# Kernel tuning notes

Hardware: AMD Instinct MI355X
Metric: run time of the kernel (lower is better)

The kernel has to match this reference:

```python
import jax, jax.numpy as jnp
import numpy as np

N_MAPS = 6          # n: maps per class (5 kernels + 1 text)
N_CLASSES = 2       # len(text_classify)
RATIO = 3
LAMBDA = 0.7
EPS = 1e-4
NEG_INF = -1e30


def setup_inputs() -> dict:
    key = jax.random.key(0)
    k1, k2, k3 = jax.random.split(key, 3)
    B, C, H, W = 8, N_CLASSES * N_MAPS, 640, 640
    outputs = jax.random.normal(k1, (B, C, H, W), dtype=jnp.float32)
    labels = jax.random.uniform(k2, (B, C, H, W), dtype=jnp.float32)
    training_mask = jax.random.uniform(k3, (B, 1, H, W), dtype=jnp.float32)
    return {"outputs": outputs, "labels": labels, "training_mask": training_mask}


def _dice_loss(pred, target, mask):
    # pred/target: (B, HW) or (B, K, HW); mask broadcastable. sums over last axis.
    p = jax.nn.sigmoid(pred) * mask
    t = target * mask
    a = jnp.sum(p * t, axis=-1)
    b = jnp.sum(p * p, axis=-1) + EPS
    c = jnp.sum(t * t, axis=-1) + EPS
    return 1.0 - 2.0 * a / (b + c)


def _ohem_single(score, gt, tm):
    # score/gt/tm: (H, W). Returns float32 (H, W) selection mask.
    pos_num = jnp.sum((gt > 0.5) & (tm > 0.5))
    neg = gt <= 0.5
    neg_total = jnp.sum(neg)
    neg_num = jnp.minimum(pos_num * RATIO, neg_total)
    # descending sort of negative-position scores
    neg_sorted = -jnp.sort(-jnp.where(neg, score, NEG_INF).ravel())
    thr = neg_sorted[jnp.clip(neg_num - 1, 0, score.size - 1)]
    sel = ((score >= thr) | (gt > 0.5)) & (tm > 0.5)
    fallback = (pos_num == 0) | (neg_num == 0)
    return jnp.where(fallback, tm, sel.astype(jnp.float32))


def reference(outputs, labels, training_mask):
    B, C, H, W = outputs.shape
    tm = training_mask[:, 0]  # (B, H, W)
    text_losses, kernel_losses, class_losses = [], [], []
    for i in range(N_CLASSES):
        texts = outputs[:, (i + 1) * N_MAPS - 1]                 # (B, H, W)
        kernels = outputs[:, i * N_MAPS:(i + 1) * N_MAPS - 1]    # (B, K, H, W)
        gt_texts = labels[:, (i + 1) * N_MAPS - 1]
        gt_kernels = labels[:, i * N_MAPS:(i + 1) * N_MAPS - 1]
        # OHEM mask (detached in original via numpy round-trip)
        sel_text = jax.lax.stop_gradient(jax.vmap(_ohem_single)(texts, gt_texts, tm))
        loss_text = _dice_loss(texts.reshape(B, -1), gt_texts.reshape(B, -1),
                               sel_text.reshape(B, -1))  # (B,)
        # kernel mask: (sigmoid(texts) > 0.5) & (tm > 0.5), detached
        sel_k = jax.lax.stop_gradient(
            ((jax.nn.sigmoid(texts) > 0.5) & (tm > 0.5)).astype(jnp.float32))
        K = gt_kernels.shape[1]
        loss_kernels = _dice_loss(kernels.reshape(B, K, -1),
                                  gt_kernels.reshape(B, K, -1),
                                  sel_k.reshape(B, 1, -1))  # (B, K) per-kernel losses
        loss_kernels = jnp.mean(loss_kernels, axis=1)  # mean over kernels -> (B,)
        lt = jnp.mean(loss_text)      # reduction='mean'
        lk = jnp.mean(loss_kernels)
        loss = LAMBDA * lt + (1.0 - LAMBDA) * lk
        text_losses.append(lt)
        kernel_losses.append(lk)
        class_losses.append(loss)
    muti_class_loss_avg = jnp.mean(jnp.stack(class_losses))
    text_loss_avg = jnp.mean(jnp.stack(text_losses))
    kernel_loss_avg = jnp.mean(jnp.stack(kernel_losses))
    # stacked as (3,): [muti_class_loss_avg, text_loss_avg, kernel_loss_avg]
    return jnp.stack([muti_class_loss_avg, text_loss_avg, kernel_loss_avg])
```

## Files before the change

kernel.cpp:

```cpp
#include <hip/hip_runtime.h>

#define HW 409600
#define NCH 12

#define OFF_TACC   0
#define OFF_KACC   256
#define OFF_TFAST  1280
#define OFF_TFB    1536
#define OFF_POSF   1792
#define OFF_NEGF   1856
#define OFF_DONE   1920
#define OFF_NEGNUM 1984
#define OFF_SEL1   2048
#define OFF_KREM1  2112
#define OFF_SEL2   2176
#define OFF_KREM2  2240
#define OFF_THR    2304
#define OFF_HA     4096
#define OFF_HB     (OFF_HA + 16*2048*4)
#define OFF_HC     (OFF_HB + 16*2048*4)
#define OFF_META_END (OFF_HC + 16*1024*4)
#define OFF_MASK   ((OFF_META_END + 255) & ~255)

__device__ __forceinline__ unsigned flipkey(float x){
  unsigned b = __float_as_uint(x);
  return (b & 0x80000000u) ? ~b : (b | 0x80000000u);
}
__device__ __forceinline__ float unflip(unsigned u){
  unsigned b = (u & 0x80000000u) ? (u ^ 0x80000000u) : ~u;
  return __uint_as_float(b);
}

__device__ __forceinline__ float sigm(float x){
  return __fdividef(1.0f, 1.0f + __expf(-x));
}

__global__ __launch_bounds__(256) void k_main(
    const float* __restrict__ outputs, const float* __restrict__ labels,
    const float* __restrict__ tmask, unsigned char* __restrict__ maskb,
    float* __restrict__ posF, float* __restrict__ negF,
    float* __restrict__ tfastA, float* __restrict__ tfbA,
    float* __restrict__ kaccA)
{
  int img = blockIdx.x / 200;
  int blk = blockIdx.x % 200;
  int ci = img >> 3, bi = img & 7;
  const float* ob = outputs + (size_t)(bi*NCH + ci*6)*HW;
  const float* lb = labels  + (size_t)(bi*NCH + ci*6)*HW;
  const float* mp = tmask   + (size_t)bi*HW;
  unsigned char* mw = maskb + (size_t)img*HW;

  float ka0=0,ka1=0,ka2=0,ka3=0,ka4=0;
  float kb0=0,kb1=0,kb2=0,kb3=0,kb4=0;
  float kc0=0,kc1=0,kc2=0,kc3=0,kc4=0;
  float af=0,bf=0,cf=0;
  float ab_=0,bb_=0,cb_=0;
  unsigned pos=0, neg=0;

  #pragma unroll
  for (int it=0; it<2; it++){
    int px = blk*2048 + it*1024 + (int)threadIdx.x*4;
    float4 ov0 = *(const float4*)(ob + 0*HW + px);
    float4 ov1 = *(const float4*)(ob + 1*HW + px);
    float4 ov2 = *(const float4*)(ob + 2*HW + px);
    float4 ov3 = *(const float4*)(ob + 3*HW + px);
    float4 ov4 = *(const float4*)(ob + 4*HW + px);
    float4 ov5 = *(const float4*)(ob + 5*HW + px);
    float4 lv0 = *(const float4*)(lb + 0*HW + px);
    float4 lv1 = *(const float4*)(lb + 1*HW + px);
    float4 lv2 = *(const float4*)(lb + 2*HW + px);
    float4 lv3 = *(const float4*)(lb + 3*HW + px);
    float4 lv4 = *(const float4*)(lb + 4*HW + px);
    float4 lv5 = *(const float4*)(lb + 5*HW + px);
    float4 mv  = *(const float4*)(mp + px);

    float oo[6][4] = {{ov0.x,ov0.y,ov0.z,ov0.w},{ov1.x,ov1.y,ov1.z,ov1.w},
                      {ov2.x,ov2.y,ov2.z,ov2.w},{ov3.x,ov3.y,ov3.z,ov3.w},
                      {ov4.x,ov4.y,ov4.z,ov4.w},{ov5.x,ov5.y,ov5.z,ov5.w}};
    float ll[6][4] = {{lv0.x,lv0.y,lv0.z,lv0.w},{lv1.x,lv1.y,lv1.z,lv1.w},
                      {lv2.x,lv2.y,lv2.z,lv2.w},{lv3.x,lv3.y,lv3.z,lv3.w},
                      {lv4.x,lv4.y,lv4.z,lv4.w},{lv5.x,lv5.y,lv5.z,lv5.w}};
    float tmv[4] = {mv.x,mv.y,mv.z,mv.w};
    unsigned char mby[4];

    #pragma unroll
    for (int c=0;c<4;c++){
      float t  = oo[5][c];
      float g  = ll[5][c];
      float tm = tmv[c];
      bool tpos  = (tm > 0.5f);
      bool isneg = (g <= 0.5f);
      bool selk  = (t > 0.0f) && tpos;
      pos += (unsigned)((!isneg) && tpos);
      neg += (unsigned)isneg;
      mby[c] = (unsigned char)((selk?1u:0u)|(tpos?2u:0u)|(isneg?4u:0u));

      float s5 = sigm(t);
      float mf = tpos ? 1.0f : 0.0f;
      af += mf * (s5*g);
      bf += mf * (s5*s5);
      cf += mf * (g*g);
      float pfb = s5*tm, tfb = g*tm;
      ab_ += pfb*tfb; bb_ += pfb*pfb; cb_ += tfb*tfb;
      float mk = selk ? 1.0f : 0.0f;
      {
        float s, l;
        s = sigm(oo[0][c]); l = ll[0][c];
        ka0 += mk*(s*l); kb0 += mk*(s*s); kc0 += mk*(l*l);
        s = sigm(oo[1][c]); l = ll[1][c];
        ka1 += mk*(s*l); kb1 += mk*(s*s); kc1 += mk*(l*l);
        s = sigm(oo[2][c]); l = ll[2][c];
        ka2 += mk*(s*l); kb2 += mk*(s*s); kc2 += mk*(l*l);
        s = sigm(oo[3][c]); l = ll[3][c];
        ka3 += mk*(s*l); kb3 += mk*(s*s); kc3 += mk*(l*l);
        s = sigm(oo[4][c]); l = ll[4][c];
        ka4 += mk*(s*l); kb4 += mk*(s*s); kc4 += mk*(l*l);
      }
    }
    *(uchar4*)(mw + px) = make_uchar4(mby[0],mby[1],mby[2],mby[3]);
  }

  float red[23] = {af,bf,cf, ab_,bb_,cb_,
                   ka0,kb0,kc0, ka1,kb1,kc1, ka2,kb2,kc2,
                   ka3,kb3,kc3, ka4,kb4,kc4,
                   (float)pos, (float)neg};
  #pragma unroll
  for (int k=0;k<23;k++){
    #pragma unroll
    for (int o=32;o;o>>=1) red[k] += __shfl_down(red[k],o,64);
  }
  __shared__ float sred[4][23];
  int wv = threadIdx.x >> 6, ln = threadIdx.x & 63;
  if (ln==0){
    #pragma unroll
    for (int k=0;k<23;k++) sred[wv][k] = red[k];
  }
  __syncthreads();
  int t = threadIdx.x;
  if (t < 23){
    float v = sred[0][t]+sred[1][t]+sred[2][t]+sred[3][t];
    float* dst;
    if      (t < 3)  dst = tfastA + img*3 + t;
    else if (t < 6)  dst = tfbA   + img*3 + (t-3);
    else if (t < 21) dst = kaccA  + img*15 + (t-6);
    else if (t ==21) dst = posF + img;
    else             dst = negF + img;
    atomicAdd(dst, v);
  }
}

__global__ void k_decide(
    const float* __restrict__ posF, const float* __restrict__ negF,
    const float* __restrict__ tfastA, const float* __restrict__ tfbA,
    float* __restrict__ tacc, unsigned* __restrict__ doneA,
    unsigned* __restrict__ negnumA, float* __restrict__ thrA)
{
  int img = threadIdx.x;
  if (img >= 16) return;
  float pos = posF[img], negt = negF[img];
  float nn = fminf(pos*3.0f, negt);
  bool fb   = (pos == 0.0f) || (nn == 0.0f);
  bool fast = (!fb) && (nn == negt);
  thrA[img] = 0.0f;
  if (fb || fast){
    doneA[img] = 1u; negnumA[img] = 1u;
    const float* src = fb ? (tfbA + img*3) : (tfastA + img*3);
    tacc[img*3+0] = src[0];
    tacc[img*3+1] = src[1];
    tacc[img*3+2] = src[2];
  } else {
    doneA[img] = 0u;
    negnumA[img] = (unsigned)(nn + 0.5f);
  }
}


__global__ __launch_bounds__(256) void k_hista(
    const float* __restrict__ outputs, const unsigned char* __restrict__ maskb,
    const unsigned* __restrict__ doneA, unsigned* __restrict__ histA)
{
  int img = blockIdx.x / 50;
  if (doneA[img]) return;
  int blk = blockIdx.x % 50;
  int ci = img>>3, bi = img&7;
  const float* tp = outputs + (size_t)(bi*NCH + ci*6 + 5)*HW;
  const unsigned char* mk = maskb + (size_t)img*HW;
  __shared__ unsigned lh[2048];
  for (int j=threadIdx.x; j<2048; j+=256) lh[j]=0u;
  __syncthreads();
  #pragma unroll
  for (int it=0; it<8; it++){
    int px = blk*8192 + it*1024 + (int)threadIdx.x*4;
    float4 tv = *(const float4*)(tp+px);
    uchar4 mq = *(const uchar4*)(mk+px);
    float tt[4]={tv.x,tv.y,tv.z,tv.w};
    unsigned char ma[4]={mq.x,mq.y,mq.z,mq.w};
    #pragma unroll
    for (int c=0;c<4;c++)
      if (ma[c] & 4) atomicAdd(&lh[flipkey(tt[c]) >> 21], 1u);
  }
  __syncthreads();
  unsigned* gh = histA + (size_t)img*2048u;
  for (int j=threadIdx.x; j<2048; j+=256){
    unsigned v = lh[j];
    if (v) atomicAdd(&gh[j], v);
  }
}

template<int NB>
__device__ void scan_desc(const unsigned* h, unsigned k, unsigned* selOut, unsigned* kremOut)
{
  const int PER = NB/256;
  int t = threadIdx.x;
  unsigned s=0;
  #pragma unroll
  for (int j=0;j<PER;j++) s += h[t*PER+j];
  __shared__ unsigned cs[256];
  cs[t]=s; __syncthreads();
  if (t==0){
    unsigned cum=0, ch=0, kin=k;
    for (int c=255;c>=0;c--){
      if (cum + cs[c] >= k){ ch=(unsigned)c; kin=k-cum; break; }
      cum += cs[c];
    }
    unsigned cum2=0, sel=ch*PER, kr=1;
    for (int x=PER-1;x>=0;x--){
      unsigned v = h[ch*PER+x];
      cum2 += v;
      if (cum2 >= kin){ sel=ch*PER+(unsigned)x; kr = kin - (cum2 - v); break; }
    }
    *selOut = sel; *kremOut = kr;
  }
}

__global__ __launch_bounds__(256) void k_scan_a(
    const unsigned* __restrict__ histA, const unsigned* __restrict__ doneA,
    const unsigned* __restrict__ negnumA, unsigned* __restrict__ sel1A,
    unsigned* __restrict__ krem1A)
{
  int img = blockIdx.x;
  if (doneA[img]) return;
  scan_desc<2048>(histA + (size_t)img*2048u, negnumA[img], &sel1A[img], &krem1A[img]);
}

__global__ __launch_bounds__(256) void k_histb(
    const float* __restrict__ outputs, const unsigned char* __restrict__ maskb,
    const unsigned* __restrict__ sel1A, const unsigned* __restrict__ doneA,
    unsigned* __restrict__ histB)
{
  int img = blockIdx.x / 50;
  if (doneA[img]) return;
  int blk = blockIdx.x % 50;
  int ci = img>>3, bi = img&7;
  unsigned sel1 = sel1A[img];
  const float* tp = outputs + (size_t)(bi*NCH + ci*6 + 5)*HW;
  const unsigned char* mk = maskb + (size_t)img*HW;
  __shared__ unsigned lh[2048];
  for (int j=threadIdx.x; j<2048; j+=256) lh[j]=0u;
  __syncthreads();
  #pragma unroll
  for (int it=0; it<8; it++){
    int px = blk*8192 + it*1024 + (int)threadIdx.x*4;
    float4 tv = *(const float4*)(tp+px);
    uchar4 mq = *(const uchar4*)(mk+px);
    float tt[4]={tv.x,tv.y,tv.z,tv.w};
    unsigned char ma[4]={mq.x,mq.y,mq.z,mq.w};
    #pragma unroll
    for (int c=0;c<4;c++){
      if (ma[c] & 4){
        unsigned key = flipkey(tt[c]);
        if ((key>>21) == sel1) atomicAdd(&lh[(key>>10) & 0x7FFu], 1u);
      }
    }
  }
  __syncthreads();
  unsigned* gh = histB + (size_t)img*2048u;
  for (int j=threadIdx.x; j<2048; j+=256){
    unsigned v = lh[j];
    if (v) atomicAdd(&gh[j], v);
  }
}

__global__ __launch_bounds__(256) void k_scan_b(
    const unsigned* __restrict__ histB, const unsigned* __restrict__ krem1A,
    const unsigned* __restrict__ doneA, unsigned* __restrict__ sel2A,
    unsigned* __restrict__ krem2A)
{
  int img = blockIdx.x;
  if (doneA[img]) return;
  scan_desc<2048>(histB + (size_t)img*2048u, krem1A[img], &sel2A[img], &krem2A[img]);
}

__global__ __launch_bounds__(256) void k_histc(
    const float* __restrict__ outputs, const unsigned char* __restrict__ maskb,
    const unsigned* __restrict__ sel1A, const unsigned* __restrict__ sel2A,
    const unsigned* __restrict__ doneA, unsigned* __restrict__ histC)
{
  int img = blockIdx.x / 50;
  if (doneA[img]) return;
  int blk = blockIdx.x % 50;
  int ci = img>>3, bi = img&7;
  unsigned p22 = (sel1A[img]<<11) | sel2A[img];
  const float* tp = outputs + (size_t)(bi*NCH + ci*6 + 5)*HW;
  const unsigned char* mk = maskb + (size_t)img*HW;
  __shared__ unsigned lh[1024];
  for (int j=threadIdx.x; j<1024; j+=256) lh[j]=0u;
  __syncthreads();
  #pragma unroll
  for (int it=0; it<8; it++){
    int px = blk*8192 + it*1024 + (int)threadIdx.x*4;
    float4 tv = *(const float4*)(tp+px);
    uchar4 mq = *(const uchar4*)(mk+px);
    float tt[4]={tv.x,tv.y,tv.z,tv.w};
    unsigned char ma[4]={mq.x,mq.y,mq.z,mq.w};
    #pragma unroll
    for (int c=0;c<4;c++){
      if (ma[c] & 4){
        unsigned key = flipkey(tt[c]);
        if ((key>>10) == p22) atomicAdd(&lh[key & 0x3FFu], 1u);
      }
    }
  }
  __syncthreads();
  unsigned* gh = histC + (size_t)img*1024u;
  for (int j=threadIdx.x; j<1024; j+=256){
    unsigned v = lh[j];
    if (v) atomicAdd(&gh[j], v);
  }
}

__global__ __launch_bounds__(256) void k_scan_c(
    const unsigned* __restrict__ histC, const unsigned* __restrict__ sel1A,
    const unsigned* __restrict__ sel2A, const unsigned* __restrict__ krem2A,
    const unsigned* __restrict__ doneA, float* __restrict__ thrA)
{
  int img = blockIdx.x;
  if (doneA[img]) return;
  __shared__ unsigned sel3, kr;
  scan_desc<1024>(histC + (size_t)img*1024u, krem2A[img], &sel3, &kr);
  __syncthreads();
  if (threadIdx.x==0){
    unsigned key = (sel1A[img]<<21) | (sel2A[img]<<10) | sel3;
    thrA[img] = unflip(key);
  }
}

__global__ __launch_bounds__(256) void k_dtext(
    const float* __restrict__ outputs, const float* __restrict__ labels,
    const unsigned char* __restrict__ maskb, const unsigned* __restrict__ doneA,
    const float* __restrict__ thrA, float* __restrict__ tacc)
{
  int img = blockIdx.x / 50;
  if (doneA[img]) return;
  int blk = blockIdx.x % 50;
  int ci = img>>3, bi = img&7;
  const float* tp = outputs + (size_t)(bi*NCH + ci*6 + 5)*HW;
  const float* gp = labels  + (size_t)(bi*NCH + ci*6 + 5)*HW;
  const unsigned char* mk = maskb + (size_t)img*HW;
  float thr = thrA[img];
  float sa=0.f, sb=0.f, sc=0.f;
  #pragma unroll
  for (int half=0; half<2; half++){
    int base = blk*8192 + half*4096 + (int)threadIdx.x*4;
    float4 pv0 = *(const float4*)(tp+base);
    float4 pv1 = *(const float4*)(tp+base+1024);
    float4 pv2 = *(const float4*)(tp+base+2048);
    float4 pv3 = *(const float4*)(tp+base+3072);
    float4 gv0 = *(const float4*)(gp+base);
    float4 gv1 = *(const float4*)(gp+base+1024);
    float4 gv2 = *(const float4*)(gp+base+2048);
    float4 gv3 = *(const float4*)(gp+base+3072);
    uchar4 mq0 = *(const uchar4*)(mk+base);
    uchar4 mq1 = *(const uchar4*)(mk+base+1024);
    uchar4 mq2 = *(const uchar4*)(mk+base+2048);
    uchar4 mq3 = *(const uchar4*)(mk+base+3072);
    float pa[16]={pv0.x,pv0.y,pv0.z,pv0.w, pv1.x,pv1.y,pv1.z,pv1.w,
                  pv2.x,pv2.y,pv2.z,pv2.w, pv3.x,pv3.y,pv3.z,pv3.w};
    float ga[16]={gv0.x,gv0.y,gv0.z,gv0.w, gv1.x,gv1.y,gv1.z,gv1.w,
                  gv2.x,gv2.y,gv2.z,gv2.w, gv3.x,gv3.y,gv3.z,gv3.w};
    unsigned char ma[16]={mq0.x,mq0.y,mq0.z,mq0.w, mq1.x,mq1.y,mq1.z,mq1.w,
                          mq2.x,mq2.y,mq2.z,mq2.w, mq3.x,mq3.y,mq3.z,mq3.w};
    #pragma unroll
    for (int c=0;c<16;c++){
      float m = (((pa[c] >= thr) || (ga[c] > 0.5f)) && (ma[c] & 2)) ? 1.0f : 0.0f;
      float p = sigm(pa[c]) * m;
      float tt = ga[c]*m;
      sa += p*tt; sb += p*p; sc += tt*tt;
    }
  }
  #pragma unroll
  for (int o=32;o;o>>=1){
    sa += __shfl_down(sa,o,64); sb += __shfl_down(sb,o,64); sc += __shfl_down(sc,o,64);
  }
  __shared__ float ra[4], rb[4], rc[4];
  int wv = threadIdx.x>>6, ln = threadIdx.x&63;
  if (ln==0){ ra[wv]=sa; rb[wv]=sb; rc[wv]=sc; }
  __syncthreads();
  if (threadIdx.x==0){
    float* acc = tacc + img*3;
    atomicAdd(acc+0, ra[0]+ra[1]+ra[2]+ra[3]);
    atomicAdd(acc+1, rb[0]+rb[1]+rb[2]+rb[3]);
    atomicAdd(acc+2, rc[0]+rc[1]+rc[2]+rc[3]);
  }
}

__global__ void k_final(const float* __restrict__ tacc, const float* __restrict__ kacc,
                        float* __restrict__ out)
{
  if (blockIdx.x==0 && threadIdx.x==0){
    const float EPSF = 1e-4f;
    float ltA[2], lkA[2];
    for (int i=0;i<2;i++){
      float lt=0.f;
      for (int b=0;b<8;b++){
        int img=i*8+b;
        float a=tacc[img*3], p2=tacc[img*3+1]+EPSF, t2=tacc[img*3+2]+EPSF;
        lt += 1.f - 2.f*a/(p2+t2);
      }
      lt *= 0.125f;
      float lk=0.f;
      for (int b=0;b<8;b++) for (int k=0;k<5;k++){
        int idx=((i*8+b)*5+k)*3;
        float a=kacc[idx], p2=kacc[idx+1]+EPSF, t2=kacc[idx+2]+EPSF;
        lk += 1.f - 2.f*a/(p2+t2);
      }
      lk /= 40.f;
      ltA[i]=lt; lkA[i]=lk;
    }
    float l0 = 0.7f*ltA[0] + 0.3f*lkA[0];
    float l1 = 0.7f*ltA[1] + 0.3f*lkA[1];
    out[0]=0.5f*(l0+l1);
    out[1]=0.5f*(ltA[0]+ltA[1]);
    out[2]=0.5f*(lkA[0]+lkA[1]);
  }
}

extern "C" void kernel_launch(void* const* d_in, const int* in_sizes, int n_in,
                              void* d_out, int out_size, void* d_ws, size_t ws_size,
                              hipStream_t stream)
{
  const float* outputs = (const float*)d_in[0];
  const float* labels  = (const float*)d_in[1];
  const float* tmask   = (const float*)d_in[2];
  float* out = (float*)d_out;
  char* ws = (char*)d_ws;
  float* tacc      = (float*)(ws + OFF_TACC);
  float* kacc      = (float*)(ws + OFF_KACC);
  float* tfastA    = (float*)(ws + OFF_TFAST);
  float* tfbA      = (float*)(ws + OFF_TFB);
  float* posF      = (float*)(ws + OFF_POSF);
  float* negF      = (float*)(ws + OFF_NEGF);
  unsigned* doneA  = (unsigned*)(ws + OFF_DONE);
  unsigned* negnumA= (unsigned*)(ws + OFF_NEGNUM);
  unsigned* sel1A  = (unsigned*)(ws + OFF_SEL1);
  unsigned* krem1A = (unsigned*)(ws + OFF_KREM1);
  unsigned* sel2A  = (unsigned*)(ws + OFF_SEL2);
  unsigned* krem2A = (unsigned*)(ws + OFF_KREM2);
  float* thrA      = (float*)(ws + OFF_THR);
  unsigned* histA  = (unsigned*)(ws + OFF_HA);
  unsigned* histB  = (unsigned*)(ws + OFF_HB);
  unsigned* histC  = (unsigned*)(ws + OFF_HC);
  unsigned char* maskb = (unsigned char*)(ws + OFF_MASK);

  hipMemsetAsync(ws, 0, OFF_META_END, stream);
  k_main  <<<3200,256,0,stream>>>(outputs, labels, tmask, maskb, posF, negF,
                                  tfastA, tfbA, kacc);
  k_decide<<<1,64,0,stream>>>(posF, negF, tfastA, tfbA, tacc, doneA, negnumA, thrA);
  k_hista <<<800,256,0,stream>>>(outputs, maskb, doneA, histA);
  k_scan_a<<<16,256,0,stream>>>(histA, doneA, negnumA, sel1A, krem1A);
  k_histb <<<800,256,0,stream>>>(outputs, maskb, sel1A, doneA, histB);
  k_scan_b<<<16,256,0,stream>>>(histB, krem1A, doneA, sel2A, krem2A);
  k_histc <<<800,256,0,stream>>>(outputs, maskb, sel1A, sel2A, doneA, histC);
  k_scan_c<<<16,256,0,stream>>>(histC, sel1A, sel2A, krem2A, doneA, thrA);
  k_dtext <<<800,256,0,stream>>>(outputs, labels, maskb, doneA, thrA, tacc);
  k_final <<<1,64,0,stream>>>(tacc, kacc, out);
}
```

Before: 353.3 us.

## Fuse OHEM select and dice tail into one cooperative kernel, drop mask buffer

Replaces the chain of decide, three histogram passes, three scans, text-dice and final kernels with a single cooperative kernel that uses grid-wide syncs between phases. When every image takes the fast or fallback path it returns right after the decide phase. The per-pixel byte mask buffer is removed: later passes re-read labels and the training mask in place of the packed mask. The main kernel now handles one chunk per block with twice as many blocks. This cuts launch overhead and the mask write traffic, at the cost of extra float reads in the tail phases and a tail grid of only 256 blocks.

```diff
diff --git a/kernel.cpp b/kernel.cpp
--- a/kernel.cpp
+++ b/kernel.cpp
@@ -1,4 +1,6 @@
 #include <hip/hip_runtime.h>
+#include <hip/hip_cooperative_groups.h>
+namespace cg = cooperative_groups;
 
 #define HW 409600
 #define NCH 12
@@ -16,11 +18,10 @@
 #define OFF_SEL2   2176
 #define OFF_KREM2  2240
 #define OFF_THR    2304
+#define OFF_ANYG   2368
 #define OFF_HA     4096
 #define OFF_HB     (OFF_HA + 16*2048*4)
 #define OFF_HC     (OFF_HB + 16*2048*4)
-#define OFF_META_END (OFF_HC + 16*1024*4)
-#define OFF_MASK   ((OFF_META_END + 255) & ~255)
 
 __device__ __forceinline__ unsigned flipkey(float x){
   unsigned b = __float_as_uint(x);
@@ -30,25 +31,46 @@
   unsigned b = (u & 0x80000000u) ? (u ^ 0x80000000u) : ~u;
   return __uint_as_float(b);
 }
-
 __device__ __forceinline__ float sigm(float x){
   return __fdividef(1.0f, 1.0f + __expf(-x));
 }
 
 __global__ __launch_bounds__(256) void k_main(
     const float* __restrict__ outputs, const float* __restrict__ labels,
-    const float* __restrict__ tmask, unsigned char* __restrict__ maskb,
+    const float* __restrict__ tmask,
     float* __restrict__ posF, float* __restrict__ negF,
     float* __restrict__ tfastA, float* __restrict__ tfbA,
     float* __restrict__ kaccA)
 {
-  int img = blockIdx.x / 200;
-  int blk = blockIdx.x % 200;
+  int img = blockIdx.x / 400;
+  int blk = blockIdx.x % 400;
   int ci = img >> 3, bi = img & 7;
   const float* ob = outputs + (size_t)(bi*NCH + ci*6)*HW;
   const float* lb = labels  + (size_t)(bi*NCH + ci*6)*HW;
   const float* mp = tmask   + (size_t)bi*HW;
-  unsigned char* mw = maskb + (size_t)img*HW;
+  int px = blk*1024 + (int)threadIdx.x*4;
+
+  float4 ov0 = *(const float4*)(ob + 0*HW + px);
+  float4 ov1 = *(const float4*)(ob + 1*HW + px);
+  float4 ov2 = *(const float4*)(ob + 2*HW + px);
+  float4 ov3 = *(const float4*)(ob + 3*HW + px);
+  float4 ov4 = *(const float4*)(ob + 4*HW + px);
+  float4 ov5 = *(const float4*)(ob + 5*HW + px);
+  float4 lv0 = *(const float4*)(lb + 0*HW + px);
+  float4 lv1 = *(const float4*)(lb + 1*HW + px);
+  float4 lv2 = *(const float4*)(lb + 2*HW + px);
+  float4 lv3 = *(const float4*)(lb + 3*HW + px);
+  float4 lv4 = *(const float4*)(lb + 4*HW + px);
+  float4 lv5 = *(const float4*)(lb + 5*HW + px);
+  float4 mv  = *(const float4*)(mp + px);
+
+  float oo[6][4] = {{ov0.x,ov0.y,ov0.z,ov0.w},{ov1.x,ov1.y,ov1.z,ov1.w},
+                    {ov2.x,ov2.y,ov2.z,ov2.w},{ov3.x,ov3.y,ov3.z,ov3.w},
+                    {ov4.x,ov4.y,ov4.z,ov4.w},{ov5.x,ov5.y,ov5.z,ov5.w}};
+  float ll[6][4] = {{lv0.x,lv0.y,lv0.z,lv0.w},{lv1.x,lv1.y,lv1.z,lv1.w},
+                    {lv2.x,lv2.y,lv2.z,lv2.w},{lv3.x,lv3.y,lv3.z,lv3.w},
+                    {lv4.x,lv4.y,lv4.z,lv4.w},{lv5.x,lv5.y,lv5.z,lv5.w}};
+  float tmv[4] = {mv.x,mv.y,mv.z,mv.w};
 
   float ka0=0,ka1=0,ka2=0,ka3=0,ka4=0;
   float kb0=0,kb1=0,kb2=0,kb3=0,kb4=0;
@@ -58,66 +80,37 @@
   unsigned pos=0, neg=0;
 
   #pragma unroll
-  for (int it=0; it<2; it++){
-    int px = blk*2048 + it*1024 + (int)threadIdx.x*4;
-    float4 ov0 = *(const float4*)(ob + 0*HW + px);
-    float4 ov1 = *(const float4*)(ob + 1*HW + px);
-    float4 ov2 = *(const float4*)(ob + 2*HW + px);
-    float4 ov3 = *(const float4*)(ob + 3*HW + px);
-    float4 ov4 = *(const float4*)(ob + 4*HW + px);
-    float4 ov5 = *(const float4*)(ob + 5*HW + px);
-    float4 lv0 = *(const float4*)(lb + 0*HW + px);
-    float4 lv1 = *(const float4*)(lb + 1*HW + px);
-    float4 lv2 = *(const float4*)(lb + 2*HW + px);
-    float4 lv3 = *(const float4*)(lb + 3*HW + px);
-    float4 lv4 = *(const float4*)(lb + 4*HW + px);
-    float4 lv5 = *(const float4*)(lb + 5*HW + px);
-    float4 mv  = *(const float4*)(mp + px);
-
-    float oo[6][4] = {{ov0.x,ov0.y,ov0.z,ov0.w},{ov1.x,ov1.y,ov1.z,ov1.w},
-                      {ov2.x,ov2.y,ov2.z,ov2.w},{ov3.x,ov3.y,ov3.z,ov3.w},
-                      {ov4.x,ov4.y,ov4.z,ov4.w},{ov5.x,ov5.y,ov5.z,ov5.w}};
-    float ll[6][4] = {{lv0.x,lv0.y,lv0.z,lv0.w},{lv1.x,lv1.y,lv1.z,lv1.w},
-                      {lv2.x,lv2.y,lv2.z,lv2.w},{lv3.x,lv3.y,lv3.z,lv3.w},
-                      {lv4.x,lv4.y,lv4.z,lv4.w},{lv5.x,lv5.y,lv5.z,lv5.w}};
-    float tmv[4] = {mv.x,mv.y,mv.z,mv.w};
-    unsigned char mby[4];
-
-    #pragma unroll
-    for (int c=0;c<4;c++){
-      float t  = oo[5][c];
-      float g  = ll[5][c];
-      float tm = tmv[c];
-      bool tpos  = (tm > 0.5f);
-      bool isneg = (g <= 0.5f);
-      bool selk  = (t > 0.0f) && tpos;
-      pos += (unsigned)((!isneg) && tpos);
-      neg += (unsigned)isneg;
-      mby[c] = (unsigned char)((selk?1u:0u)|(tpos?2u:0u)|(isneg?4u:0u));
-
-      float s5 = sigm(t);
-      float mf = tpos ? 1.0f : 0.0f;
-      af += mf * (s5*g);
-      bf += mf * (s5*s5);
-      cf += mf * (g*g);
-      float pfb = s5*tm, tfb = g*tm;
-      ab_ += pfb*tfb; bb_ += pfb*pfb; cb_ += tfb*tfb;
-      float mk = selk ? 1.0f : 0.0f;
-      {
-        float s, l;
-        s = sigm(oo[0][c]); l = ll[0][c];
-        ka0 += mk*(s*l); kb0 += mk*(s*s); kc0 += mk*(l*l);
-        s = sigm(oo[1][c]); l = ll[1][c];
-        ka1 += mk*(s*l); kb1 += mk*(s*s); kc1 += mk*(l*l);
-        s = sigm(oo[2][c]); l = ll[2][c];
-        ka2 += mk*(s*l); kb2 += mk*(s*s); kc2 += mk*(l*l);
-        s = sigm(oo[3][c]); l = ll[3][c];
-        ka3 += mk*(s*l); kb3 += mk*(s*s); kc3 += mk*(l*l);
-        s = sigm(oo[4][c]); l = ll[4][c];
-        ka4 += mk*(s*l); kb4 += mk*(s*s); kc4 += mk*(l*l);
-      }
-    }
-    *(uchar4*)(mw + px) = make_uchar4(mby[0],mby[1],mby[2],mby[3]);
+  for (int c=0;c<4;c++){
+    float t  = oo[5][c];
+    float g  = ll[5][c];
+    float tm = tmv[c];
+    bool tpos  = (tm > 0.5f);
+    bool isneg = (g <= 0.5f);
+    bool selk  = (t > 0.0f) && tpos;
+    pos += (unsigned)((!isneg) && tpos);
+    neg += (unsigned)isneg;
+
+    float s5 = sigm(t);
+    float mf = tpos ? 1.0f : 0.0f;
+    af += mf * (s5*g);
+    bf += mf * (s5*s5);
+    cf += mf * (g*g);
+    float pfb = s5*tm, tfb = g*tm;
+    ab_ += pfb*tfb; bb_ += pfb*pfb; cb_ += tfb*tfb;
+    float mk = selk ? 1.0f : 0.0f;
+    {
+      float s, l;
+      s = sigm(oo[0][c]); l = ll[0][c];
+      ka0 += mk*(s*l); kb0 += mk*(s*s); kc0 += mk*(l*l);
+      s = sigm(oo[1][c]); l = ll[1][c];
+      ka1 += mk*(s*l); kb1 += mk*(s*s); kc1 += mk*(l*l);
+      s = sigm(oo[2][c]); l = ll[2][c];
+      ka2 += mk*(s*l); kb2 += mk*(s*s); kc2 += mk*(l*l);
+      s = sigm(oo[3][c]); l = ll[3][c];
+      ka3 += mk*(s*l); kb3 += mk*(s*s); kc3 += mk*(l*l);
+      s = sigm(oo[4][c]); l = ll[4][c];
+      ka4 += mk*(s*l); kb4 += mk*(s*s); kc4 += mk*(l*l);
+    }
   }
 
   float red[23] = {af,bf,cf, ab_,bb_,cb_,
@@ -146,64 +139,6 @@
     else if (t ==21) dst = posF + img;
     else             dst = negF + img;
     atomicAdd(dst, v);
-  }
-}
-
-__global__ void k_decide(
-    const float* __restrict__ posF, const float* __restrict__ negF,
-    const float* __restrict__ tfastA, const float* __restrict__ tfbA,
-    float* __restrict__ tacc, unsigned* __restrict__ doneA,
-    unsigned* __restrict__ negnumA, float* __restrict__ thrA)
-{
-  int img = threadIdx.x;
-  if (img >= 16) return;
-  float pos = posF[img], negt = negF[img];
-  float nn = fminf(pos*3.0f, negt);
-  bool fb   = (pos == 0.0f) || (nn == 0.0f);
-  bool fast = (!fb) && (nn == negt);
-  thrA[img] = 0.0f;
-  if (fb || fast){
-    doneA[img] = 1u; negnumA[img] = 1u;
-    const float* src = fb ? (tfbA + img*3) : (tfastA + img*3);
-    tacc[img*3+0] = src[0];
-    tacc[img*3+1] = src[1];
-    tacc[img*3+2] = src[2];
-  } else {
-    doneA[img] = 0u;
-    negnumA[img] = (unsigned)(nn + 0.5f);
-  }
-}
-
-
-__global__ __launch_bounds__(256) void k_hista(
-    const float* __restrict__ outputs, const unsigned char* __restrict__ maskb,
-    const unsigned* __restrict__ doneA, unsigned* __restrict__ histA)
-{
-  int img = blockIdx.x / 50;
-  if (doneA[img]) return;
-  int blk = blockIdx.x % 50;
-  int ci = img>>3, bi = img&7;
-  const float* tp = outputs + (size_t)(bi*NCH + ci*6 + 5)*HW;
-  const unsigned char* mk = maskb + (size_t)img*HW;
-  __shared__ unsigned lh[2048];
-  for (int j=threadIdx.x; j<2048; j+=256) lh[j]=0u;
-  __syncthreads();
-  #pragma unroll
-  for (int it=0; it<8; it++){
-    int px = blk*8192 + it*1024 + (int)threadIdx.x*4;
-    float4 tv = *(const float4*)(tp+px);
-    uchar4 mq = *(const uchar4*)(mk+px);
-    float tt[4]={tv.x,tv.y,tv.z,tv.w};
-    unsigned char ma[4]={mq.x,mq.y,mq.z,mq.w};
-    #pragma unroll
-    for (int c=0;c<4;c++)
-      if (ma[c] & 4) atomicAdd(&lh[flipkey(tt[c]) >> 21], 1u);
-  }
-  __syncthreads();
-  unsigned* gh = histA + (size_t)img*2048u;
-  for (int j=threadIdx.x; j<2048; j+=256){
-    unsigned v = lh[j];
-    if (v) atomicAdd(&gh[j], v);
   }
 }
 
@@ -231,219 +166,42 @@
     }
     *selOut = sel; *kremOut = kr;
   }
-}
-
-__global__ __launch_bounds__(256) void k_scan_a(
-    const unsigned* __restrict__ histA, const unsigned* __restrict__ doneA,
-    const unsigned* __restrict__ negnumA, unsigned* __restrict__ sel1A,
-    unsigned* __restrict__ krem1A)
+  __syncthreads();
+}
+
+__device__ void do_final(const float* tacc, const float* kacc, float* out)
 {
-  int img = blockIdx.x;
-  if (doneA[img]) return;
-  scan_desc<2048>(histA + (size_t)img*2048u, negnumA[img], &sel1A[img], &krem1A[img]);
-}
-
-__global__ __launch_bounds__(256) void k_histb(
-    const float* __restrict__ outputs, const unsigned char* __restrict__ maskb,
-    const unsigned* __restrict__ sel1A, const unsigned* __restrict__ doneA,
-    unsigned* __restrict__ histB)
+  const float EPSF = 1e-4f;
+  float ltA[2], lkA[2];
+  for (int i=0;i<2;i++){
+    float lt=0.f;
+    for (int b=0;b<8;b++){
+      int img=i*8+b;
+      float a=tacc[img*3], p2=tacc[img*3+1]+EPSF, t2=tacc[img*3+2]+EPSF;
+      lt += 1.f - 2.f*a/(p2+t2);
+    }
+    lt *= 0.125f;
+    float lk=0.f;
+    for (int b=0;b<8;b++) for (int k=0;k<5;k++){
+      int idx=((i*8+b)*5+k)*3;
+      float a=kacc[idx], p2=kacc[idx+1]+EPSF, t2=kacc[idx+2]+EPSF;
+      lk += 1.f - 2.f*a/(p2+t2);
+    }
+    lk /= 40.f;
+    ltA[i]=lt; lkA[i]=lk;
+  }
+  float l0 = 0.7f*ltA[0] + 0.3f*lkA[0];
+  float l1 = 0.7f*ltA[1] + 0.3f*lkA[1];
+  out[0]=0.5f*(l0+l1);
+  out[1]=0.5f*(ltA[0]+ltA[1]);
+  out[2]=0.5f*(lkA[0]+lkA[1]);
+}
+
+__global__ __launch_bounds__(256) void k_tail(
+    const float* __restrict__ outputs, const float* __restrict__ labels,
+    const float* __restrict__ tmask, char* __restrict__ ws, float* __restrict__ out)
 {
-  int img = blockIdx.x / 50;
-  if (doneA[img]) return;
-  int blk = blockIdx.x % 50;
-  int ci = img>>3, bi = img&7;
-  unsigned sel1 = sel1A[img];
-  const float* tp = outputs + (size_t)(bi*NCH + ci*6 + 5)*HW;
-  const unsigned char* mk = maskb + (size_t)img*HW;
-  __shared__ unsigned lh[2048];
-  for (int j=threadIdx.x; j<2048; j+=256) lh[j]=0u;
-  __syncthreads();
-  #pragma unroll
-  for (int it=0; it<8; it++){
-    int px = blk*8192 + it*1024 + (int)threadIdx.x*4;
-    float4 tv = *(const float4*)(tp+px);
-    uchar4 mq = *(const uchar4*)(mk+px);
-    float tt[4]={tv.x,tv.y,tv.z,tv.w};
-    unsigned char ma[4]={mq.x,mq.y,mq.z,mq.w};
-    #pragma unroll
-    for (int c=0;c<4;c++){
-      if (ma[c] & 4){
-        unsigned key = flipkey(tt[c]);
-        if ((key>>21) == sel1) atomicAdd(&lh[(key>>10) & 0x7FFu], 1u);
-      }
-    }
-  }
-  __syncthreads();
-  unsigned* gh = histB + (size_t)img*2048u;
-  for (int j=threadIdx.x; j<2048; j+=256){
-    unsigned v = lh[j];
-    if (v) atomicAdd(&gh[j], v);
-  }
-}
-
-__global__ __launch_bounds__(256) void k_scan_b(
-    const unsigned* __restrict__ histB, const unsigned* __restrict__ krem1A,
-    const unsigned* __restrict__ doneA, unsigned* __restrict__ sel2A,
-    unsigned* __restrict__ krem2A)
-{
-  int img = blockIdx.x;
-  if (doneA[img]) return;
-  scan_desc<2048>(histB + (size_t)img*2048u, krem1A[img], &sel2A[img], &krem2A[img]);
-}
-
-__global__ __launch_bounds__(256) void k_histc(
-    const float* __restrict__ outputs, const unsigned char* __restrict__ maskb,
-    const unsigned* __restrict__ sel1A, const unsigned* __restrict__ sel2A,
-    const unsigned* __restrict__ doneA, unsigned* __restrict__ histC)
-{
-  int img = blockIdx.x / 50;
-  if (doneA[img]) return;
-  int blk = blockIdx.x % 50;
-  int ci = img>>3, bi = img&7;
-  unsigned p22 = (sel1A[img]<<11) | sel2A[img];
-  const float* tp = outputs + (size_t)(bi*NCH + ci*6 + 5)*HW;
-  const unsigned char* mk = maskb + (size_t)img*HW;
-  __shared__ unsigned lh[1024];
-  for (int j=threadIdx.x; j<1024; j+=256) lh[j]=0u;
-  __syncthreads();
-  #pragma unroll
-  for (int it=0; it<8; it++){
-    int px = blk*8192 + it*1024 + (int)threadIdx.x*4;
-    float4 tv = *(const float4*)(tp+px);
-    uchar4 mq = *(const uchar4*)(mk+px);
-    float tt[4]={tv.x,tv.y,tv.z,tv.w};
-    unsigned char ma[4]={mq.x,mq.y,mq.z,mq.w};
-    #pragma unroll
-    for (int c=0;c<4;c++){
-      if (ma[c] & 4){
-        unsigned key = flipkey(tt[c]);
-        if ((key>>10) == p22) atomicAdd(&lh[key & 0x3FFu], 1u);
-      }
-    }
-  }
-  __syncthreads();
-  unsigned* gh = histC + (size_t)img*1024u;
-  for (int j=threadIdx.x; j<1024; j+=256){
-    unsigned v = lh[j];
-    if (v) atomicAdd(&gh[j], v);
-  }
-}
-
-__global__ __launch_bounds__(256) void k_scan_c(
-    const unsigned* __restrict__ histC, const unsigned* __restrict__ sel1A,
-    const unsigned* __restrict__ sel2A, const unsigned* __restrict__ krem2A,
-    const unsigned* __restrict__ doneA, float* __restrict__ thrA)
-{
-  int img = blockIdx.x;
-  if (doneA[img]) return;
-  __shared__ unsigned sel3, kr;
-  scan_desc<1024>(histC + (size_t)img*1024u, krem2A[img], &sel3, &kr);
-  __syncthreads();
-  if (threadIdx.x==0){
-    unsigned key = (sel1A[img]<<21) | (sel2A[img]<<10) | sel3;
-    thrA[img] = unflip(key);
-  }
-}
-
-__global__ __launch_bounds__(256) void k_dtext(
-    const float* __restrict__ outputs, const float* __restrict__ labels,
-    const unsigned char* __restrict__ maskb, const unsigned* __restrict__ doneA,
-    const float* __restrict__ thrA, float* __restrict__ tacc)
-{
-  int img = blockIdx.x / 50;
-  if (doneA[img]) return;
-  int blk = blockIdx.x % 50;
-  int ci = img>>3, bi = img&7;
-  const float* tp = outputs + (size_t)(bi*NCH + ci*6 + 5)*HW;
-  const float* gp = labels  + (size_t)(bi*NCH + ci*6 + 5)*HW;
-  const unsigned char* mk = maskb + (size_t)img*HW;
-  float thr = thrA[img];
-  float sa=0.f, sb=0.f, sc=0.f;
-  #pragma unroll
-  for (int half=0; half<2; half++){
-    int base = blk*8192 + half*4096 + (int)threadIdx.x*4;
-    float4 pv0 = *(const float4*)(tp+base);
-    float4 pv1 = *(const float4*)(tp+base+1024);
-    float4 pv2 = *(const float4*)(tp+base+2048);
-    float4 pv3 = *(const float4*)(tp+base+3072);
-    float4 gv0 = *(const float4*)(gp+base);
-    float4 gv1 = *(const float4*)(gp+base+1024);
-    float4 gv2 = *(const float4*)(gp+base+2048);
-    float4 gv3 = *(const float4*)(gp+base+3072);
-    uchar4 mq0 = *(const uchar4*)(mk+base);
-    uchar4 mq1 = *(const uchar4*)(mk+base+1024);
-    uchar4 mq2 = *(const uchar4*)(mk+base+2048);
-    uchar4 mq3 = *(const uchar4*)(mk+base+3072);
-    float pa[16]={pv0.x,pv0.y,pv0.z,pv0.w, pv1.x,pv1.y,pv1.z,pv1.w,
-                  pv2.x,pv2.y,pv2.z,pv2.w, pv3.x,pv3.y,pv3.z,pv3.w};
-    float ga[16]={gv0.x,gv0.y,gv0.z,gv0.w, gv1.x,gv1.y,gv1.z,gv1.w,
-                  gv2.x,gv2.y,gv2.z,gv2.w, gv3.x,gv3.y,gv3.z,gv3.w};
-    unsigned char ma[16]={mq0.x,mq0.y,mq0.z,mq0.w, mq1.x,mq1.y,mq1.z,mq1.w,
-                          mq2.x,mq2.y,mq2.z,mq2.w, mq3.x,mq3.y,mq3.z,mq3.w};
-    #pragma unroll
-    for (int c=0;c<16;c++){
-      float m = (((pa[c] >= thr) || (ga[c] > 0.5f)) && (ma[c] & 2)) ? 1.0f : 0.0f;
-      float p = sigm(pa[c]) * m;
-      float tt = ga[c]*m;
-      sa += p*tt; sb += p*p; sc += tt*tt;
-    }
-  }
-  #pragma unroll
-  for (int o=32;o;o>>=1){
-    sa += __shfl_down(sa,o,64); sb += __shfl_down(sb,o,64); sc += __shfl_down(sc,o,64);
-  }
-  __shared__ float ra[4], rb[4], rc[4];
-  int wv = threadIdx.x>>6, ln = threadIdx.x&63;
-  if (ln==0){ ra[wv]=sa; rb[wv]=sb; rc[wv]=sc; }
-  __syncthreads();
-  if (threadIdx.x==0){
-    float* acc = tacc + img*3;
-    atomicAdd(acc+0, ra[0]+ra[1]+ra[2]+ra[3]);
-    atomicAdd(acc+1, rb[0]+rb[1]+rb[2]+rb[3]);
-    atomicAdd(acc+2, rc[0]+rc[1]+rc[2]+rc[3]);
-  }
-}
-
-__global__ void k_final(const float* __restrict__ tacc, const float* __restrict__ kacc,
-                        float* __restrict__ out)
-{
-  if (blockIdx.x==0 && threadIdx.x==0){
-    const float EPSF = 1e-4f;
-    float ltA[2], lkA[2];
-    for (int i=0;i<2;i++){
-      float lt=0.f;
-      for (int b=0;b<8;b++){
-        int img=i*8+b;
-        float a=tacc[img*3], p2=tacc[img*3+1]+EPSF, t2=tacc[img*3+2]+EPSF;
-        lt += 1.f - 2.f*a/(p2+t2);
-      }
-      lt *= 0.125f;
-      float lk=0.f;
-      for (int b=0;b<8;b++) for (int k=0;k<5;k++){
-        int idx=((i*8+b)*5+k)*3;
-        float a=kacc[idx], p2=kacc[idx+1]+EPSF, t2=kacc[idx+2]+EPSF;
-        lk += 1.f - 2.f*a/(p2+t2);
-      }
-      lk /= 40.f;
-      ltA[i]=lt; lkA[i]=lk;
-    }
-    float l0 = 0.7f*ltA[0] + 0.3f*lkA[0];
-    float l1 = 0.7f*ltA[1] + 0.3f*lkA[1];
-    out[0]=0.5f*(l0+l1);
-    out[1]=0.5f*(ltA[0]+ltA[1]);
-    out[2]=0.5f*(lkA[0]+lkA[1]);
-  }
-}
-
-extern "C" void kernel_launch(void* const* d_in, const int* in_sizes, int n_in,
-                              void* d_out, int out_size, void* d_ws, size_t ws_size,
-                              hipStream_t stream)
-{
-  const float* outputs = (const float*)d_in[0];
-  const float* labels  = (const float*)d_in[1];
-  const float* tmask   = (const float*)d_in[2];
-  float* out = (float*)d_out;
-  char* ws = (char*)d_ws;
+  cg::grid_group grid = cg::this_grid();
   float* tacc      = (float*)(ws + OFF_TACC);
   float* kacc      = (float*)(ws + OFF_KACC);
   float* tfastA    = (float*)(ws + OFF_TFAST);
@@ -457,21 +215,231 @@
   unsigned* sel2A  = (unsigned*)(ws + OFF_SEL2);
   unsigned* krem2A = (unsigned*)(ws + OFF_KREM2);
   float* thrA      = (float*)(ws + OFF_THR);
+  unsigned* anyG   = (unsigned*)(ws + OFF_ANYG);
   unsigned* histA  = (unsigned*)(ws + OFF_HA);
   unsigned* histB  = (unsigned*)(ws + OFF_HB);
   unsigned* histC  = (unsigned*)(ws + OFF_HC);
-  unsigned char* maskb = (unsigned char*)(ws + OFF_MASK);
-
-  hipMemsetAsync(ws, 0, OFF_META_END, stream);
-  k_main  <<<3200,256,0,stream>>>(outputs, labels, tmask, maskb, posF, negF,
-                                  tfastA, tfbA, kacc);
-  k_decide<<<1,64,0,stream>>>(posF, negF, tfastA, tfbA, tacc, doneA, negnumA, thrA);
-  k_hista <<<800,256,0,stream>>>(outputs, maskb, doneA, histA);
-  k_scan_a<<<16,256,0,stream>>>(histA, doneA, negnumA, sel1A, krem1A);
-  k_histb <<<800,256,0,stream>>>(outputs, maskb, sel1A, doneA, histB);
-  k_scan_b<<<16,256,0,stream>>>(histB, krem1A, doneA, sel2A, krem2A);
-  k_histc <<<800,256,0,stream>>>(outputs, maskb, sel1A, sel2A, doneA, histC);
-  k_scan_c<<<16,256,0,stream>>>(histC, sel1A, sel2A, krem2A, doneA, thrA);
-  k_dtext <<<800,256,0,stream>>>(outputs, labels, maskb, doneA, thrA, tacc);
-  k_final <<<1,64,0,stream>>>(tacc, kacc, out);
-}
+
+  if (blockIdx.x == 0){
+    int t = threadIdx.x;
+    unsigned d = 1u;
+    if (t < 16){
+      float pos = posF[t], negt = negF[t];
+      float nn = fminf(pos*3.0f, negt);
+      bool fb   = (pos == 0.0f) || (nn == 0.0f);
+      bool fast = (!fb) && (nn == negt);
+      d = (fb || fast) ? 1u : 0u;
+      doneA[t] = d;
+      negnumA[t] = d ? 1u : (unsigned)(nn + 0.5f);
+      thrA[t] = 0.0f;
+      if (d){
+        const float* src = fb ? (tfbA + t*3) : (tfastA + t*3);
+        tacc[t*3+0] = src[0];
+        tacc[t*3+1] = src[1];
+        tacc[t*3+2] = src[2];
+      }
+    }
+    unsigned long long nd = __ballot((t < 16) && (d == 0u));
+    if (t == 0) anyG[0] = (nd != 0ull) ? 1u : 0u;
+    __threadfence();
+  }
+  grid.sync();
+
+  if (anyG[0] == 0u){
+    if (blockIdx.x == 0 && threadIdx.x == 0) do_final(tacc, kacc, out);
+    return;
+  }
+
+  for (int i = blockIdx.x*256 + threadIdx.x; i < 81920; i += gridDim.x*256)
+    histA[i] = 0u;
+  grid.sync();
+
+  __shared__ unsigned lh[2048];
+
+  for (int tile = blockIdx.x; tile < 800; tile += gridDim.x){
+    int img = tile/50;
+    if (doneA[img]) continue;
+    int blk = tile%50;
+    int ci = img>>3, bi = img&7;
+    const float* tp = outputs + (size_t)(bi*NCH + ci*6 + 5)*HW;
+    const float* gp = labels  + (size_t)(bi*NCH + ci*6 + 5)*HW;
+    for (int j=threadIdx.x; j<2048; j+=256) lh[j]=0u;
+    __syncthreads();
+    for (int it=0; it<8; it++){
+      int px = blk*8192 + it*1024 + (int)threadIdx.x*4;
+      float4 tv = *(const float4*)(tp+px);
+      float4 gv = *(const float4*)(gp+px);
+      float tt[4]={tv.x,tv.y,tv.z,tv.w};
+      float gg[4]={gv.x,gv.y,gv.z,gv.w};
+      #pragma unroll
+      for (int c=0;c<4;c++)
+        if (gg[c] <= 0.5f) atomicAdd(&lh[flipkey(tt[c]) >> 21], 1u);
+    }
+    __syncthreads();
+    unsigned* gh = histA + (size_t)img*2048u;
+    for (int j=threadIdx.x; j<2048; j+=256){
+      unsigned v = lh[j];
+      if (v) atomicAdd(&gh[j], v);
+    }
+    __syncthreads();
+  }
+  grid.sync();
+
+  if (blockIdx.x < 16 && !doneA[blockIdx.x])
+    scan_desc<2048>(histA + (size_t)blockIdx.x*2048u, negnumA[blockIdx.x],
+                    &sel1A[blockIdx.x], &krem1A[blockIdx.x]);
+  grid.sync();
+
+  for (int tile = blockIdx.x; tile < 800; tile += gridDim.x){
+    int img = tile/50;
+    if (doneA[img]) continue;
+    int blk = tile%50;
+    int ci = img>>3, bi = img&7;
+    unsigned sel1 = sel1A[img];
+    const float* tp = outputs + (size_t)(bi*NCH + ci*6 + 5)*HW;
+    const float* gp = labels  + (size_t)(bi*NCH + ci*6 + 5)*HW;
+    for (int j=threadIdx.x; j<2048; j+=256) lh[j]=0u;
+    __syncthreads();
+    for (int it=0; it<8; it++){
+      int px = blk*8192 + it*1024 + (int)threadIdx.x*4;
+      float4 tv = *(const float4*)(tp+px);
+      float4 gv = *(const float4*)(gp+px);
+      float tt[4]={tv.x,tv.y,tv.z,tv.w};
+      float gg[4]={gv.x,gv.y,gv.z,gv.w};
+      #pragma unroll
+      for (int c=0;c<4;c++){
+        if (gg[c] <= 0.5f){
+          unsigned key = flipkey(tt[c]);
+          if ((key>>21) == sel1) atomicAdd(&lh[(key>>10) & 0x7FFu], 1u);
+        }
+      }
+    }
+    __syncthreads();
+    unsigned* gh = histB + (size_t)img*2048u;
+    for (int j=threadIdx.x; j<2048; j+=256){
+      unsigned v = lh[j];
+      if (v) atomicAdd(&gh[j], v);
+    }
+    __syncthreads();
+  }
+  grid.sync();
+
+  if (blockIdx.x < 16 && !doneA[blockIdx.x])
+    scan_desc<2048>(histB + (size_t)blockIdx.x*2048u, krem1A[blockIdx.x],
+                    &sel2A[blockIdx.x], &krem2A[blockIdx.x]);
+  grid.sync();
+
+  for (int tile = blockIdx.x; tile < 800; tile += gridDim.x){
+    int img = tile/50;
+    if (doneA[img]) continue;
+    int blk = tile%50;
+    int ci = img>>3, bi = img&7;
+    unsigned p22 = (sel1A[img]<<11) | sel2A[img];
+    const float* tp = outputs + (size_t)(bi*NCH + ci*6 + 5)*HW;
+    const float* gp = labels  + (size_t)(bi*NCH + ci*6 + 5)*HW;
+    for (int j=threadIdx.x; j<1024; j+=256) lh[j]=0u;
+    __syncthreads();
+    for (int it=0; it<8; it++){
+      int px = blk*8192 + it*1024 + (int)threadIdx.x*4;
+      float4 tv = *(const float4*)(tp+px);
+      float4 gv = *(const float4*)(gp+px);
+      float tt[4]={tv.x,tv.y,tv.z,tv.w};
+      float gg[4]={gv.x,gv.y,gv.z,gv.w};
+      #pragma unroll
+      for (int c=0;c<4;c++){
+        if (gg[c] <= 0.5f){
+          unsigned key = flipkey(tt[c]);
+          if ((key>>10) == p22) atomicAdd(&lh[key & 0x3FFu], 1u);
+        }
+      }
+    }
+    __syncthreads();
+    unsigned* gh = histC + (size_t)img*1024u;
+    for (int j=threadIdx.x; j<1024; j+=256){
+      unsigned v = lh[j];
+      if (v) atomicAdd(&gh[j], v);
+    }
+    __syncthreads();
+  }
+  grid.sync();
+
+  if (blockIdx.x < 16 && !doneA[blockIdx.x]){
+    __shared__ unsigned sel3, kr;
+    scan_desc<1024>(histC + (size_t)blockIdx.x*1024u, krem2A[blockIdx.x], &sel3, &kr);
+    if (threadIdx.x==0){
+      unsigned key = (sel1A[blockIdx.x]<<21) | (sel2A[blockIdx.x]<<10) | sel3;
+      thrA[blockIdx.x] = unflip(key);
+    }
+  }
+  grid.sync();
+
+  for (int tile = blockIdx.x; tile < 800; tile += gridDim.x){
+    int img = tile/50;
+    if (doneA[img]) continue;
+    int blk = tile%50;
+    int ci = img>>3, bi = img&7;
+    const float* tp = outputs + (size_t)(bi*NCH + ci*6 + 5)*HW;
+    const float* gp = labels  + (size_t)(bi*NCH + ci*6 + 5)*HW;
+    const float* mp = tmask   + (size_t)bi*HW;
+    float thr = thrA[img];
+    float sa=0.f, sb=0.f, sc=0.f;
+    for (int it=0; it<8; it++){
+      int px = blk*8192 + it*1024 + (int)threadIdx.x*4;
+      float4 pv = *(const float4*)(tp+px);
+      float4 gv = *(const float4*)(gp+px);
+      float4 mv = *(const float4*)(mp+px);
+      float pa[4]={pv.x,pv.y,pv.z,pv.w};
+      float ga[4]={gv.x,gv.y,gv.z,gv.w};
+      float ma[4]={mv.x,mv.y,mv.z,mv.w};
+      #pragma unroll
+      for (int c=0;c<4;c++){
+        float m = (((pa[c] >= thr) || (ga[c] > 0.5f)) && (ma[c] > 0.5f)) ? 1.0f : 0.0f;
+        float p = sigm(pa[c]) * m;
+        float tt = ga[c]*m;
+        sa += p*tt; sb += p*p; sc += tt*tt;
+      }
+    }
+    #pragma unroll
+    for (int o=32;o;o>>=1){
+      sa += __shfl_down(sa,o,64); sb += __shfl_down(sb,o,64); sc += __shfl_down(sc,o,64);
+    }
+    __shared__ float ra[4], rb[4], rc[4];
+    int wv = threadIdx.x>>6, ln = threadIdx.x&63;
+    if (ln==0){ ra[wv]=sa; rb[wv]=sb; rc[wv]=sc; }
+    __syncthreads();
+    if (threadIdx.x==0){
+      float* acc = tacc + img*3;
+      atomicAdd(acc+0, ra[0]+ra[1]+ra[2]+ra[3]);
+      atomicAdd(acc+1, rb[0]+rb[1]+rb[2]+rb[3]);
+      atomicAdd(acc+2, rc[0]+rc[1]+rc[2]+rc[3]);
+    }
+    __syncthreads();
+  }
+  grid.sync();
+
+  if (blockIdx.x == 0 && threadIdx.x == 0) do_final(tacc, kacc, out);
+}
+
+extern "C" void kernel_launch(void* const* d_in, const int* in_sizes, int n_in,
+                              void* d_out, int out_size, void* d_ws, size_t ws_size,
+                              hipStream_t stream)
+{
+  const float* outputs = (const float*)d_in[0];
+  const float* labels  = (const float*)d_in[1];
+  const float* tmask   = (const float*)d_in[2];
+  float* out = (float*)d_out;
+  char* ws = (char*)d_ws;
+  float* posF      = (float*)(ws + OFF_POSF);
+  float* negF      = (float*)(ws + OFF_NEGF);
+  float* tfastA    = (float*)(ws + OFF_TFAST);
+  float* tfbA      = (float*)(ws + OFF_TFB);
+  float* kacc      = (float*)(ws + OFF_KACC);
+
+  hipMemsetAsync(ws, 0, 2048, stream);
+  k_main<<<6400,256,0,stream>>>(outputs, labels, tmask, posF, negF,
+                                tfastA, tfbA, kacc);
+  void* args[] = { (void*)&outputs, (void*)&labels, (void*)&tmask,
+                   (void*)&ws, (void*)&out };
+  hipLaunchCooperativeKernel((const void*)k_tail, dim3(256), dim3(256),
+                             args, 0, stream);
+}
```

Result: slower. 392.9 us (+11.2%).
